# Performance work log

Measured on AMD Instinct MI355X. Metric: run time of the kernel, lower is better.

## Reference

```python
import jax, jax.numpy as jnp
import numpy as np

# PlatonicConv (graph mode, attention=True, use_key=True): tetrahedron group G=12
G = 12
H_EFF = 2          # num_heads // G = 24 // 12
HEAD_D = 16        # embed_dim_g // H_EFF = (384//12) // 2
GH = G * H_EFF     # 24
IN_C = 384
EMB = 384
OUT_C = 384
N_GRAPHS = 32
NODES_PER_GRAPH = 64
N = N_GRAPHS * NODES_PER_GRAPH   # 2048
SPATIAL = 3


def _fc_edges():
    # fully-connected edges within each graph (batch[src]==batch[dst]), incl. self loops
    n = NODES_PER_GRAPH
    offs = np.arange(N_GRAPHS, dtype=np.int32) * n
    gs, gd = np.meshgrid(np.arange(n, dtype=np.int32), np.arange(n, dtype=np.int32), indexing='ij')
    src = (offs[:, None] + gs.reshape(-1)[None, :]).reshape(-1)
    dst = (offs[:, None] + gd.reshape(-1)[None, :]).reshape(-1)
    return jnp.asarray(src), jnp.asarray(dst)


def setup_inputs() -> dict:
    key = jax.random.key(0)
    ks = jax.random.split(key, 12)
    sw = 1.0 / np.sqrt(IN_C)
    x = jax.random.normal(ks[0], (N, IN_C), jnp.float32)
    pos = jax.random.normal(ks[1], (N, SPATIAL), jnp.float32)
    Wq = jax.random.normal(ks[2], (IN_C, EMB), jnp.float32) * sw
    bq = jnp.zeros((EMB,), jnp.float32)
    Wk = jax.random.normal(ks[3], (IN_C, EMB), jnp.float32) * sw
    bk = jnp.zeros((EMB,), jnp.float32)
    Wv = jax.random.normal(ks[4], (IN_C, EMB), jnp.float32) * sw
    bv = jnp.zeros((EMB,), jnp.float32)
    Wo = jax.random.normal(ks[5], (EMB, OUT_C), jnp.float32) * (1.0 / np.sqrt(EMB))
    bo = jnp.zeros((OUT_C,), jnp.float32)
    # RoPE frequencies: freq_sigma=1.0, random init, per spatial dim / head / half-dim
    rope_freqs = jax.random.normal(ks[6], (SPATIAL, H_EFF, HEAD_D // 2), jnp.float32)
    src, dst = _fc_edges()
    return {"x": x, "pos": pos, "Wq": Wq, "bq": bq, "Wk": Wk, "bk": bk,
            "Wv": Wv, "bv": bv, "Wo": Wo, "bo": bo, "rope_freqs": rope_freqs,
            "src": src, "dst": dst}


def _rope(t, pos, freqs):
    # t: [N, G, H, D]; pos: [N, 3]; freqs: [3, H, D//2]
    theta = jnp.einsum('ns,shf->nhf', pos, freqs)            # [N, H, D/2]
    cos = jnp.cos(theta)[:, None, :, :]                      # broadcast over G
    sin = jnp.sin(theta)[:, None, :, :]
    tr = t.reshape(t.shape[:-1] + (HEAD_D // 2, 2))
    t1, t2 = tr[..., 0], tr[..., 1]
    rot = jnp.stack([t1 * cos - t2 * sin, t1 * sin + t2 * cos], axis=-1)
    return rot.reshape(t.shape)


def reference(x, pos, Wq, bq, Wk, bk, Wv, bv, Wo, bo, rope_freqs, src, dst):
    n = x.shape[0]
    q = (x @ Wq + bq).reshape(n, G, H_EFF, HEAD_D)
    k = (x @ Wk + bk).reshape(n, G, H_EFF, HEAD_D)
    v = (x @ Wv + bv).reshape(n, G, H_EFF, HEAD_D)
    q = _rope(q, pos, rope_freqs)
    k = _rope(k, pos, rope_freqs)
    qf = q.reshape(n, GH, HEAD_D)
    kf = k.reshape(n, GH, HEAD_D)
    vf = v.reshape(n, GH, HEAD_D)
    # gather by edge index
    q_src = qf[src]                                          # [E, GH, D]
    k_dst = kf[dst]
    v_dst = vf[dst]
    scores = jnp.sum(q_src * k_dst, axis=-1) * (HEAD_D ** -0.5)  # [E, GH]
    # scatter softmax over edges grouped by src node (per group-head)
    m = jax.ops.segment_max(scores, src, num_segments=n)     # [N, GH]
    ex = jnp.exp(scores - m[src])
    den = jax.ops.segment_sum(ex, src, num_segments=n)
    a = ex / den[src]                                        # [E, GH]
    out = jax.ops.segment_sum(a[..., None] * v_dst, src, num_segments=n)  # [N, GH, D]
    out = out.reshape(n, GH * HEAD_D)
    return out @ Wo + bo
```

## Files before the change

### kernel.cpp

```cpp
#include <hip/hip_runtime.h>


#define NNODES   2048
#define KDIM     384
#define NGRAPHS  32
#define NPG      64
#define GHEADS   24
#define HDIM     16

typedef __attribute__((ext_vector_type(8))) short short8;
typedef __attribute__((ext_vector_type(4))) float f32x4;

__device__ __forceinline__ short f2bf(float f) {
    unsigned u = __builtin_bit_cast(unsigned, f);
    u += 0x7FFFu + ((u >> 16) & 1u);
    return (short)(u >> 16);
}

__global__ __launch_bounds__(256) void prep_kernel(
    const float* __restrict__ x,
    const float* __restrict__ Wq, const float* __restrict__ Wk,
    const float* __restrict__ Wv, const float* __restrict__ Wo,
    short* __restrict__ WT, short* __restrict__ xb)
{
    const int b   = blockIdx.x;
    const int tid = threadIdx.x;
    if (b < 576) {
        __shared__ float tile[32][33];
        const int mat = b / 144;
        const int t   = b - mat * 144;
        const int k0  = (t / 12) * 32;
        const int n0  = (t % 12) * 32;
        const float* W = (mat == 0) ? Wq : (mat == 1) ? Wk : (mat == 2) ? Wv : Wo;
        const int cx = tid & 31;
        const int ty = tid >> 5;
        #pragma unroll
        for (int i = 0; i < 4; ++i) {
            const int rr = ty + 8 * i;
            tile[rr][cx] = W[(size_t)(k0 + rr) * KDIM + n0 + cx];
        }
        __syncthreads();
        #pragma unroll
        for (int i = 0; i < 4; ++i) {
            const int rr = ty + 8 * i;
            WT[(size_t)(mat * 384 + n0 + rr) * KDIM + k0 + cx] = f2bf(tile[cx][rr]);
        }
    } else {
        const int idx = ((b - 576) * 256 + tid) * 8;
        const f32x4* xp = reinterpret_cast<const f32x4*>(x + idx);
        f32x4 v0 = xp[0], v1 = xp[1];
        short8 o;
        o[0] = f2bf(v0[0]); o[1] = f2bf(v0[1]); o[2] = f2bf(v0[2]); o[3] = f2bf(v0[3]);
        o[4] = f2bf(v1[0]); o[5] = f2bf(v1[1]); o[6] = f2bf(v1[2]); o[7] = f2bf(v1[3]);
        *reinterpret_cast<short8*>(xb + idx) = o;
    }
}

__global__ __launch_bounds__(256) void qkv_attn_kernel(
    const short* __restrict__ xb,
    const short* __restrict__ WT,
    const float* __restrict__ bq, const float* __restrict__ bk,
    const float* __restrict__ bv,
    const float* __restrict__ pos, const float* __restrict__ freqs,
    short* __restrict__ attn_out)
{
    const int blk  = blockIdx.x;
    const int gr   = blk / GHEADS;
    const int gh   = blk - gr * GHEADS;
    const int tid  = threadIdx.x;
    const int w    = tid >> 6;
    const int lane = tid & 63;
    const int fr   = lane & 15;
    const int hi   = lane >> 4;

    const short* aP  = xb + (size_t)(gr * 64 + w * 16 + fr) * KDIM + hi * 8;
    const short* bqP = WT + (size_t)(gh * 16 + fr) * KDIM + hi * 8;
    const short* bkP = bqP + (size_t)384 * KDIM;
    const short* bvP = bkP + (size_t)384 * KDIM;

    f32x4 acc[3];
    acc[0] = (f32x4){0.f, 0.f, 0.f, 0.f};
    acc[1] = acc[0];
    acc[2] = acc[0];

    #pragma unroll 4
    for (int kt = 0; kt < KDIM; kt += 32) {
        short8 af = *reinterpret_cast<const short8*>(aP + kt);
        short8 b0 = *reinterpret_cast<const short8*>(bqP + kt);
        short8 b1 = *reinterpret_cast<const short8*>(bkP + kt);
        short8 b2 = *reinterpret_cast<const short8*>(bvP + kt);
        acc[0] = __builtin_amdgcn_mfma_f32_16x16x32_bf16(af, b0, acc[0], 0, 0, 0);
        acc[1] = __builtin_amdgcn_mfma_f32_16x16x32_bf16(af, b1, acc[1], 0, 0, 0);
        acc[2] = __builtin_amdgcn_mfma_f32_16x16x32_bf16(af, b2, acc[2], 0, 0, 0);
    }

    __shared__ float q_lds[64][20];
    __shared__ float k_lds[64][20];
    __shared__ float v_lds[64][20];

    const float bias_q = bq[gh * 16 + fr];
    const float bias_k = bk[gh * 16 + fr];
    const float bias_v = bv[gh * 16 + fr];
    const int   h = gh & 1;
    const int   f = fr >> 1;
    const float F0 = freqs[h * 8 + f];
    const float F1 = freqs[16 + h * 8 + f];
    const float F2 = freqs[32 + h * 8 + f];

    #pragma unroll
    for (int rr = 0; rr < 4; ++rr) {
        const int row  = w * 16 + hi * 4 + rr;
        const int grow = gr * 64 + row;
        float qv = acc[0][rr] + bias_q;
        float kv = acc[1][rr] + bias_k;
        float vv = acc[2][rr] + bias_v;
        const float th = pos[grow * 3] * F0 + pos[grow * 3 + 1] * F1
                       + pos[grow * 3 + 2] * F2;
        const float cs = __cosf(th);
        const float sn = __sinf(th);
        const float qo = __shfl_xor(qv, 1, 64);
        const float ko = __shfl_xor(kv, 1, 64);
        qv = (fr & 1) ? (qo * sn + qv * cs) : (qv * cs - qo * sn);
        kv = (fr & 1) ? (ko * sn + kv * cs) : (kv * cs - ko * sn);
        q_lds[row][fr] = qv;
        k_lds[row][fr] = kv;
        v_lds[row][fr] = vv;
    }
    __syncthreads();

    const int qrow = w * 16 + fr;
    f32x4 q0 = *reinterpret_cast<const f32x4*>(&q_lds[qrow][0]);
    f32x4 q1 = *reinterpret_cast<const f32x4*>(&q_lds[qrow][4]);
    f32x4 q2 = *reinterpret_cast<const f32x4*>(&q_lds[qrow][8]);
    f32x4 q3 = *reinterpret_cast<const f32x4*>(&q_lds[qrow][12]);

    float sc[16];
    #pragma unroll
    for (int j = 0; j < 16; ++j) {
        const float* kp = &k_lds[hi * 16 + j][0];
        f32x4 k0 = reinterpret_cast<const f32x4*>(kp)[0];
        f32x4 k1 = reinterpret_cast<const f32x4*>(kp)[1];
        f32x4 k2 = reinterpret_cast<const f32x4*>(kp)[2];
        f32x4 k3 = reinterpret_cast<const f32x4*>(kp)[3];
        float a = q0[0]*k0[0] + q0[1]*k0[1] + q0[2]*k0[2] + q0[3]*k0[3]
                + q1[0]*k1[0] + q1[1]*k1[1] + q1[2]*k1[2] + q1[3]*k1[3]
                + q2[0]*k2[0] + q2[1]*k2[1] + q2[2]*k2[2] + q2[3]*k2[3]
                + q3[0]*k3[0] + q3[1]*k3[1] + q3[2]*k3[2] + q3[3]*k3[3];
        sc[j] = a * 0.25f;
    }

    float mx = sc[0];
    #pragma unroll
    for (int j = 1; j < 16; ++j) mx = fmaxf(mx, sc[j]);
    mx = fmaxf(mx, __shfl_xor(mx, 16, 64));
    mx = fmaxf(mx, __shfl_xor(mx, 32, 64));

    float den = 0.f;
    #pragma unroll
    for (int j = 0; j < 16; ++j) {
        sc[j] = __expf(sc[j] - mx);
        den += sc[j];
    }
    den += __shfl_xor(den, 16, 64);
    den += __shfl_xor(den, 32, 64);

    float o[16];
    #pragma unroll
    for (int d = 0; d < 16; ++d) o[d] = 0.f;
    #pragma unroll
    for (int j = 0; j < 16; ++j) {
        const float p = sc[j];
        const float* vp = &v_lds[hi * 16 + j][0];
        f32x4 v0 = reinterpret_cast<const f32x4*>(vp)[0];
        f32x4 v1 = reinterpret_cast<const f32x4*>(vp)[1];
        f32x4 v2 = reinterpret_cast<const f32x4*>(vp)[2];
        f32x4 v3 = reinterpret_cast<const f32x4*>(vp)[3];
        #pragma unroll
        for (int d = 0; d < 4; ++d) {
            o[d]      += p * v0[d];
            o[4 + d]  += p * v1[d];
            o[8 + d]  += p * v2[d];
            o[12 + d] += p * v3[d];
        }
    }
    #pragma unroll
    for (int d = 0; d < 16; ++d) {
        o[d] += __shfl_xor(o[d], 16, 64);
        o[d] += __shfl_xor(o[d], 32, 64);
    }

    if (hi == 0) {
        const float inv = 1.0f / den;
        short8 r0, r1;
        #pragma unroll
        for (int d = 0; d < 8; ++d) {
            r0[d] = f2bf(o[d] * inv);
            r1[d] = f2bf(o[8 + d] * inv);
        }
        short* op = attn_out + (size_t)(gr * 64 + qrow) * KDIM + gh * 16;
        *reinterpret_cast<short8*>(op)     = r0;
        *reinterpret_cast<short8*>(op + 8) = r1;
    }
}

__global__ __launch_bounds__(64) void out_gemm_kernel(
    const short* __restrict__ A,
    const short* __restrict__ BT,
    const float* __restrict__ bias,
    float* __restrict__ C)
{
    const int r0   = blockIdx.x * 16;
    const int c0   = blockIdx.y * 64;
    const int lane = threadIdx.x;
    const int fr   = lane & 15;
    const int hi   = lane >> 4;

    const short* aP = A + (size_t)(r0 + fr) * KDIM + hi * 8;
    const short* b0P = BT + (size_t)(c0 + fr) * KDIM + hi * 8;
    const short* b1P = b0P + (size_t)16 * KDIM;
    const short* b2P = b1P + (size_t)16 * KDIM;
    const short* b3P = b2P + (size_t)16 * KDIM;

    f32x4 acc[4];
    acc[0] = (f32x4){0.f, 0.f, 0.f, 0.f};
    acc[1] = acc[0]; acc[2] = acc[0]; acc[3] = acc[0];

    #pragma unroll 4
    for (int kt = 0; kt < KDIM; kt += 32) {
        short8 af = *reinterpret_cast<const short8*>(aP + kt);
        short8 f0 = *reinterpret_cast<const short8*>(b0P + kt);
        short8 f1 = *reinterpret_cast<const short8*>(b1P + kt);
        short8 f2 = *reinterpret_cast<const short8*>(b2P + kt);
        short8 f3 = *reinterpret_cast<const short8*>(b3P + kt);
        acc[0] = __builtin_amdgcn_mfma_f32_16x16x32_bf16(af, f0, acc[0], 0, 0, 0);
        acc[1] = __builtin_amdgcn_mfma_f32_16x16x32_bf16(af, f1, acc[1], 0, 0, 0);
        acc[2] = __builtin_amdgcn_mfma_f32_16x16x32_bf16(af, f2, acc[2], 0, 0, 0);
        acc[3] = __builtin_amdgcn_mfma_f32_16x16x32_bf16(af, f3, acc[3], 0, 0, 0);
    }

    #pragma unroll
    for (int ct = 0; ct < 4; ++ct) {
        const int c  = c0 + ct * 16 + fr;
        const float bv = bias[c];
        const int rowb = r0 + hi * 4;
        #pragma unroll
        for (int rr = 0; rr < 4; ++rr)
            C[(size_t)(rowb + rr) * KDIM + c] = acc[ct][rr] + bv;
    }
}

extern "C" void kernel_launch(void* const* d_in, const int* in_sizes, int n_in,
                              void* d_out, int out_size, void* d_ws, size_t ws_size,
                              hipStream_t stream) {
    const float* x    = (const float*)d_in[0];
    const float* pos  = (const float*)d_in[1];
    const float* Wq   = (const float*)d_in[2];
    const float* bq   = (const float*)d_in[3];
    const float* Wk   = (const float*)d_in[4];
    const float* bk   = (const float*)d_in[5];
    const float* Wv   = (const float*)d_in[6];
    const float* bv   = (const float*)d_in[7];
    const float* Wo   = (const float*)d_in[8];
    const float* bo   = (const float*)d_in[9];
    const float* rope = (const float*)d_in[10];

    char* ws = (char*)d_ws;
    short* WT   = (short*)(ws);
    short* xb   = (short*)(ws + 1179648);
    short* attn = (short*)(ws + 2752512);

    prep_kernel<<<960, 256, 0, stream>>>(x, Wq, Wk, Wv, Wo, WT, xb);

    qkv_attn_kernel<<<NGRAPHS * GHEADS, 256, 0, stream>>>(
        xb, WT, bq, bk, bv, pos, rope, attn);

    {
        dim3 grid(NNODES / 16, KDIM / 64);
        out_gemm_kernel<<<grid, 64, 0, stream>>>(
            attn, WT + (size_t)1152 * KDIM, bo, (float*)d_out);
    }
}
```

Measured before the change: 113.8 us.

## Fuse bf16 prep into QKV-attention kernel, staging weight slices in LDS

Removes the separate prep kernel. Each attention block now converts its own Q/K/V weight column slice to bf16, transposes it into padded LDS, and converts x rows from fp32 to bf16 on the fly inside the MFMA loop. Only Wo is still transposed to global memory, by 144 extra blocks launched in the same grid. This saves one launch and the global round trip of the bf16 copies. In exchange, each of the 768 blocks redundantly converts its weight slice and every x row, does scattered 2-byte LDS stores, and reuses the LDS buffer behind an extra barrier.

```diff
diff --git a/kernel.cpp b/kernel.cpp
--- a/kernel.cpp
+++ b/kernel.cpp
@@ -7,6 +7,7 @@
 #define NPG      64
 #define GHEADS   24
 #define HDIM     16
+#define WSROW    392
 
 typedef __attribute__((ext_vector_type(8))) short short8;
 typedef __attribute__((ext_vector_type(4))) float f32x4;
@@ -17,66 +18,75 @@
     return (short)(u >> 16);
 }
 
-__global__ __launch_bounds__(256) void prep_kernel(
+__global__ __launch_bounds__(256) void fused_kernel(
     const float* __restrict__ x,
-    const float* __restrict__ Wq, const float* __restrict__ Wk,
-    const float* __restrict__ Wv, const float* __restrict__ Wo,
-    short* __restrict__ WT, short* __restrict__ xb)
+    const float* __restrict__ pos,
+    const float* __restrict__ Wq, const float* __restrict__ bq,
+    const float* __restrict__ Wk, const float* __restrict__ bk,
+    const float* __restrict__ Wv, const float* __restrict__ bv,
+    const float* __restrict__ Wo,
+    const float* __restrict__ freqs,
+    short* __restrict__ WoT,
+    short* __restrict__ attn_out)
 {
-    const int b   = blockIdx.x;
+    __shared__ __align__(16) char smem[3 * 16 * WSROW * 2];
     const int tid = threadIdx.x;
-    if (b < 576) {
-        __shared__ float tile[32][33];
-        const int mat = b / 144;
-        const int t   = b - mat * 144;
-        const int k0  = (t / 12) * 32;
-        const int n0  = (t % 12) * 32;
-        const float* W = (mat == 0) ? Wq : (mat == 1) ? Wk : (mat == 2) ? Wv : Wo;
+
+    if (blockIdx.x < 144) {
+        float (*tile)[33] = reinterpret_cast<float(*)[33]>(smem);
+        const int t  = blockIdx.x;
+        const int k0 = (t / 12) * 32;
+        const int n0 = (t % 12) * 32;
         const int cx = tid & 31;
         const int ty = tid >> 5;
         #pragma unroll
         for (int i = 0; i < 4; ++i) {
             const int rr = ty + 8 * i;
-            tile[rr][cx] = W[(size_t)(k0 + rr) * KDIM + n0 + cx];
+            tile[rr][cx] = Wo[(size_t)(k0 + rr) * KDIM + n0 + cx];
         }
         __syncthreads();
         #pragma unroll
         for (int i = 0; i < 4; ++i) {
             const int rr = ty + 8 * i;
-            WT[(size_t)(mat * 384 + n0 + rr) * KDIM + k0 + cx] = f2bf(tile[cx][rr]);
-        }
-    } else {
-        const int idx = ((b - 576) * 256 + tid) * 8;
-        const f32x4* xp = reinterpret_cast<const f32x4*>(x + idx);
-        f32x4 v0 = xp[0], v1 = xp[1];
-        short8 o;
-        o[0] = f2bf(v0[0]); o[1] = f2bf(v0[1]); o[2] = f2bf(v0[2]); o[3] = f2bf(v0[3]);
-        o[4] = f2bf(v1[0]); o[5] = f2bf(v1[1]); o[6] = f2bf(v1[2]); o[7] = f2bf(v1[3]);
-        *reinterpret_cast<short8*>(xb + idx) = o;
-    }
-}
-
-__global__ __launch_bounds__(256) void qkv_attn_kernel(
-    const short* __restrict__ xb,
-    const short* __restrict__ WT,
-    const float* __restrict__ bq, const float* __restrict__ bk,
-    const float* __restrict__ bv,
-    const float* __restrict__ pos, const float* __restrict__ freqs,
-    short* __restrict__ attn_out)
-{
-    const int blk  = blockIdx.x;
-    const int gr   = blk / GHEADS;
-    const int gh   = blk - gr * GHEADS;
-    const int tid  = threadIdx.x;
+            WoT[(size_t)(n0 + rr) * KDIM + k0 + cx] = f2bf(tile[cx][rr]);
+        }
+        return;
+    }
+
+    const int blk = blockIdx.x - 144;
+    const int gr  = blk / GHEADS;
+    const int gh  = blk - gr * GHEADS;
+
+    short* WS = reinterpret_cast<short*>(smem);
+    for (int task = tid; task < 1152; task += 256) {
+        const int mat = task / KDIM;
+        const int k   = task - mat * KDIM;
+        const float* W = (mat == 0) ? Wq : (mat == 1) ? Wk : Wv;
+        const float* src = W + (size_t)k * KDIM + gh * 16;
+        f32x4 w0 = reinterpret_cast<const f32x4*>(src)[0];
+        f32x4 w1 = reinterpret_cast<const f32x4*>(src)[1];
+        f32x4 w2 = reinterpret_cast<const f32x4*>(src)[2];
+        f32x4 w3 = reinterpret_cast<const f32x4*>(src)[3];
+        short* dst = WS + (size_t)mat * 16 * WSROW + k;
+        #pragma unroll
+        for (int c = 0; c < 4; ++c) {
+            dst[(c)      * WSROW] = f2bf(w0[c]);
+            dst[(c + 4)  * WSROW] = f2bf(w1[c]);
+            dst[(c + 8)  * WSROW] = f2bf(w2[c]);
+            dst[(c + 12) * WSROW] = f2bf(w3[c]);
+        }
+    }
+    __syncthreads();
+
     const int w    = tid >> 6;
     const int lane = tid & 63;
     const int fr   = lane & 15;
     const int hi   = lane >> 4;
 
-    const short* aP  = xb + (size_t)(gr * 64 + w * 16 + fr) * KDIM + hi * 8;
-    const short* bqP = WT + (size_t)(gh * 16 + fr) * KDIM + hi * 8;
-    const short* bkP = bqP + (size_t)384 * KDIM;
-    const short* bvP = bkP + (size_t)384 * KDIM;
+    const float* aRow = x + (size_t)(gr * 64 + w * 16 + fr) * KDIM + hi * 8;
+    const short* wsq = WS + (size_t)fr * WSROW + hi * 8;
+    const short* wsk = wsq + (size_t)16 * WSROW;
+    const short* wsv = wsk + (size_t)16 * WSROW;
 
     f32x4 acc[3];
     acc[0] = (f32x4){0.f, 0.f, 0.f, 0.f};
@@ -85,18 +95,23 @@
 
     #pragma unroll 4
     for (int kt = 0; kt < KDIM; kt += 32) {
-        short8 af = *reinterpret_cast<const short8*>(aP + kt);
-        short8 b0 = *reinterpret_cast<const short8*>(bqP + kt);
-        short8 b1 = *reinterpret_cast<const short8*>(bkP + kt);
-        short8 b2 = *reinterpret_cast<const short8*>(bvP + kt);
+        f32x4 a0 = *reinterpret_cast<const f32x4*>(aRow + kt);
+        f32x4 a1 = *reinterpret_cast<const f32x4*>(aRow + kt + 4);
+        short8 af;
+        af[0] = f2bf(a0[0]); af[1] = f2bf(a0[1]); af[2] = f2bf(a0[2]); af[3] = f2bf(a0[3]);
+        af[4] = f2bf(a1[0]); af[5] = f2bf(a1[1]); af[6] = f2bf(a1[2]); af[7] = f2bf(a1[3]);
+        short8 b0 = *reinterpret_cast<const short8*>(wsq + kt);
+        short8 b1 = *reinterpret_cast<const short8*>(wsk + kt);
+        short8 b2 = *reinterpret_cast<const short8*>(wsv + kt);
         acc[0] = __builtin_amdgcn_mfma_f32_16x16x32_bf16(af, b0, acc[0], 0, 0, 0);
         acc[1] = __builtin_amdgcn_mfma_f32_16x16x32_bf16(af, b1, acc[1], 0, 0, 0);
         acc[2] = __builtin_amdgcn_mfma_f32_16x16x32_bf16(af, b2, acc[2], 0, 0, 0);
     }
-
-    __shared__ float q_lds[64][20];
-    __shared__ float k_lds[64][20];
-    __shared__ float v_lds[64][20];
+    __syncthreads();
+
+    float (*q_lds)[20] = reinterpret_cast<float(*)[20]>(smem);
+    float (*k_lds)[20] = reinterpret_cast<float(*)[20]>(smem + 5120);
+    float (*v_lds)[20] = reinterpret_cast<float(*)[20]>(smem + 10240);
 
     const float bias_q = bq[gh * 16 + fr];
     const float bias_k = bk[gh * 16 + fr];
@@ -215,7 +230,7 @@
     const int fr   = lane & 15;
     const int hi   = lane >> 4;
 
-    const short* aP = A + (size_t)(r0 + fr) * KDIM + hi * 8;
+    const short* aP  = A + (size_t)(r0 + fr) * KDIM + hi * 8;
     const short* b0P = BT + (size_t)(c0 + fr) * KDIM + hi * 8;
     const short* b1P = b0P + (size_t)16 * KDIM;
     const short* b2P = b1P + (size_t)16 * KDIM;
@@ -240,7 +255,7 @@
 
     #pragma unroll
     for (int ct = 0; ct < 4; ++ct) {
-        const int c  = c0 + ct * 16 + fr;
+        const int c    = c0 + ct * 16 + fr;
         const float bv = bias[c];
         const int rowb = r0 + hi * 4;
         #pragma unroll
@@ -265,18 +280,14 @@
     const float* rope = (const float*)d_in[10];
 
     char* ws = (char*)d_ws;
-    short* WT   = (short*)(ws);
-    short* xb   = (short*)(ws + 1179648);
-    short* attn = (short*)(ws + 2752512);
-
-    prep_kernel<<<960, 256, 0, stream>>>(x, Wq, Wk, Wv, Wo, WT, xb);
-
-    qkv_attn_kernel<<<NGRAPHS * GHEADS, 256, 0, stream>>>(
-        xb, WT, bq, bk, bv, pos, rope, attn);
+    short* WoT  = (short*)(ws);
+    short* attn = (short*)(ws + 294912);
+
+    fused_kernel<<<144 + NGRAPHS * GHEADS, 256, 0, stream>>>(
+        x, pos, Wq, bq, Wk, bk, Wv, bv, Wo, rope, WoT, attn);
 
     {
         dim3 grid(NNODES / 16, KDIM / 64);
-        out_gemm_kernel<<<grid, 64, 0, stream>>>(
-            attn, WT + (size_t)1152 * KDIM, bo, (float*)d_out);
-    }
-}
+        out_gemm_kernel<<<grid, 64, 0, stream>>>(attn, WoT, bo, (float*)d_out);
+    }
+}
```

Measured after the change: 109.5 us. 3.8% less time.
